# Performance work log

Measured on AMD Instinct MI355X. Metric: run time of the kernel, lower is better.

Reference implementation:

```python
import jax, jax.numpy as jnp
import numpy as np

B, S, E, H = 2, 2048, 1024, 16
DK = E // H
THRESHOLD = 0.1


def setup_inputs() -> dict:
    key = jax.random.key(0)
    ks = jax.random.split(key, 11)
    s = 1.0 / np.sqrt(E)
    return {
        "queries": jax.random.normal(ks[0], (B, S, E), jnp.float32),
        "keys": jax.random.normal(ks[1], (B, S, E), jnp.float32),
        "values": jax.random.normal(ks[2], (B, S, E), jnp.float32),
        "Wq": jax.random.normal(ks[3], (E, E), jnp.float32) * s,
        "bq": jnp.zeros((E,), jnp.float32),
        "Wk": jax.random.normal(ks[4], (E, E), jnp.float32) * s,
        "bk": jnp.zeros((E,), jnp.float32),
        "Wv": jax.random.normal(ks[5], (E, E), jnp.float32) * s,
        "bv": jnp.zeros((E,), jnp.float32),
        "Wp": jax.random.normal(ks[6], (E, E), jnp.float32) * s,
        "bp": jnp.zeros((E,), jnp.float32),
    }


def _split(x):
    # [B,S,E] -> [B,H,S,dk]
    return x.reshape(B, S, H, DK).transpose(0, 2, 1, 3)


def reference(queries, keys, values, Wq, bq, Wk, bk, Wv, bv, Wp, bp):
    q = _split(queries @ Wq.T + bq)
    k = _split(keys @ Wk.T + bk)
    v = _split(values @ Wv.T + bv)
    logits = jnp.einsum("bhsd,bhtd->bhst", q, k) / np.sqrt(DK)
    probs = jax.nn.softmax(logits, axis=-1)                    # [B,H,S,S]
    mask = (probs > THRESHOLD).astype(probs.dtype)
    # straight-through: value = mask*probs, grads flow via (mask*probs + probs)
    thr = mask * probs - jax.lax.stop_gradient(probs) + probs
    hidden = jnp.einsum("bhst,bhtd->bhsd", thr, v)             # [B,H,S,dk]
    merged = hidden.transpose(0, 2, 1, 3).reshape(B, S, E)
    out = merged @ Wp.T + bp
    adjacency = probs.mean(axis=1)                             # avg_attn_heads=True
    return (out, adjacency)
```

## Files before the change

### kernel.cpp

```cpp
#include <hip/hip_runtime.h>
#include <cstddef>
#include <cstdint>

constexpr size_t OUT_ELEMS = (size_t)2 * 2048 * 1024;

typedef _Float16 f16_t;
typedef __attribute__((ext_vector_type(8))) _Float16 f16x8;
typedef __attribute__((ext_vector_type(4))) float f32x4;

#define SCL2      0.1803368801111204f
#define LOG2_0P1  -3.3219280948873623f

#define EXP2F(x)  __builtin_amdgcn_exp2f(x)
#define LOG2F(x)  __builtin_amdgcn_logf(x)

#define WAITV(N)  asm volatile("s_waitcnt vmcnt(" #N ")" ::: "memory")
__device__ __forceinline__ void ringbar() {
    __builtin_amdgcn_s_barrier();
    __builtin_amdgcn_sched_barrier(0);
}

__device__ __forceinline__ f32x4 mfma16(f16x8 a, f16x8 b, f32x4 c) {
    return __builtin_amdgcn_mfma_f32_16x16x32_f16(a, b, c, 0, 0, 0);
}

__device__ __forceinline__ void gload16(const void* g, void* l) {
    __builtin_amdgcn_global_load_lds(
        (const __attribute__((address_space(1))) void*)g,
        (__attribute__((address_space(3))) void*)l, 16, 0, 0);
}

__global__ __launch_bounds__(256)
void prep_kernel(const float4* __restrict__ q, const float4* __restrict__ k,
                 const float4* __restrict__ v, const float4* __restrict__ wq,
                 const float4* __restrict__ wk, const float4* __restrict__ wv,
                 const float4* __restrict__ wp,
                 unsigned short* __restrict__ xq, unsigned short* __restrict__ xk,
                 unsigned short* __restrict__ xv, unsigned short* __restrict__ wqh,
                 unsigned short* __restrict__ wkh, unsigned short* __restrict__ wvh,
                 unsigned short* __restrict__ wph)
{
    const int z = blockIdx.y;
    const int i = blockIdx.x * 256 + threadIdx.x;
    const float4* src; unsigned short* dst; int total4;
    switch (z) {
        case 0:  src = q;  dst = xq;  total4 = 1048576; break;
        case 1:  src = k;  dst = xk;  total4 = 1048576; break;
        case 2:  src = v;  dst = xv;  total4 = 1048576; break;
        case 3:  src = wq; dst = wqh; total4 = 262144;  break;
        case 4:  src = wk; dst = wkh; total4 = 262144;  break;
        case 5:  src = wv; dst = wvh; total4 = 262144;  break;
        default: src = wp; dst = wph; total4 = 262144;  break;
    }
    if (i >= total4) return;
    const float4 v4 = src[i];
    const float vv[4] = {v4.x, v4.y, v4.z, v4.w};
    unsigned short u[4];
#pragma unroll
    for (int j = 0; j < 4; ++j) {
        f16_t h = (f16_t)vv[j];
        u[j] = __builtin_bit_cast(unsigned short, h);
    }
    uint2 w;
    w.x = u[0] | ((unsigned)u[1] << 16); w.y = u[2] | ((unsigned)u[3] << 16);
    *(uint2*)(dst + (size_t)i * 4) = w;
}

template<int OUTMODE>
__global__ __launch_bounds__(512)
void gemm_mfma(const f16_t* __restrict__ A, const f16_t* __restrict__ B,
               const float* __restrict__ bias, float scaleB,
               float* __restrict__ outF, f16_t* __restrict__ outB,
               const unsigned* __restrict__ dmask)
{
    __shared__ __align__(16) char Asl[3][16384];
    __shared__ __align__(16) char Bsl[3][16384];

    const int tid = threadIdx.x;
    const int lane = tid & 63;
    const int w = tid >> 6;
    const int wm = w >> 1;
    const int wn = w & 1;
    const int n0 = blockIdx.x * 128;
    const int m0 = blockIdx.y * 128;

    if (OUTMODE == 2) {
        const int bb = m0 >> 11;
        const int st0 = (m0 & 2047) >> 6;
        unsigned dd = 0;
        for (int hh = 0; hh < 16; ++hh)
            dd |= dmask[(bb * 16 + hh) * 32 + st0] | dmask[(bb * 16 + hh) * 32 + st0 + 1];
        if (dd == 0u) {
            const int row = tid >> 2;
            const int c0 = (tid & 3) * 32;
            float* dst = outF + (size_t)(m0 + row) * 1024 + n0 + c0;
#pragma unroll
            for (int j = 0; j < 8; ++j)
                *(float4*)(dst + j * 4) = *(const float4*)(bias + n0 + c0 + j * 4);
            return;
        }
    }

    f32x4 acc[2][4] = {};

    auto stage = [&](int ki, int buf) {
        const int kt = ki * 64;
#pragma unroll
        for (int inst = 0; inst < 2; ++inst) {
            int L = inst * 8192 + tid * 16;
            int row = L >> 7;
            int k16 = ((L >> 4) & 7) ^ (row & 7);
            gload16(A + (size_t)(m0 + row) * 1024 + kt + k16 * 8,
                    Asl[buf] + inst * 8192 + w * 1024);
            gload16(B + (size_t)(n0 + row) * 1024 + kt + k16 * 8,
                    Bsl[buf] + inst * 8192 + w * 1024);
        }
    };

    stage(0, 0);

    for (int ki = 0; ki < 16; ++ki) {
        if (ki + 1 < 16) stage(ki + 1, (ki + 1) % 3);
        if (ki < 15) { WAITV(4); } else { WAITV(0); }
        ringbar();
        const char* Ab = Asl[ki % 3];
        const char* Bb = Bsl[ki % 3];
#pragma unroll
        for (int kf = 0; kf < 2; ++kf) {
            const int k16 = kf * 4 + (lane >> 4);
            f16x8 af[2], bfr[4];
#pragma unroll
            for (int mi = 0; mi < 2; ++mi) {
                int row = wm * 32 + mi * 16 + (lane & 15);
                af[mi] = *(const f16x8*)(Ab + (row << 7) + ((k16 ^ (row & 7)) << 4));
            }
#pragma unroll
            for (int ni = 0; ni < 4; ++ni) {
                int row = wn * 64 + ni * 16 + (lane & 15);
                bfr[ni] = *(const f16x8*)(Bb + (row << 7) + ((k16 ^ (row & 7)) << 4));
            }
#pragma unroll
            for (int mi = 0; mi < 2; ++mi)
#pragma unroll
                for (int ni = 0; ni < 4; ++ni)
                    acc[mi][ni] = mfma16(af[mi], bfr[ni], acc[mi][ni]);
        }
    }

    const int crow0 = wm * 32 + (lane >> 4) * 4;
    const int ccol0 = wn * 64 + (lane & 15);
#pragma unroll
    for (int mi = 0; mi < 2; ++mi) {
#pragma unroll
        for (int ni = 0; ni < 4; ++ni) {
            const int n = n0 + ccol0 + ni * 16;
            const float bb = bias[n];
            if (OUTMODE == 2) {
#pragma unroll
                for (int r = 0; r < 4; ++r) {
                    const int m = m0 + crow0 + mi * 16 + r;
                    outF[(size_t)m * 1024 + n] = acc[mi][ni][r] + bb;
                }
            } else if (OUTMODE == 0) {
                const int h = n >> 6, d = n & 63;
#pragma unroll
                for (int r = 0; r < 4; ++r) {
                    const int m = m0 + crow0 + mi * 16 + r;
                    const int b = m >> 11, s = m & 2047;
                    const float v = acc[mi][ni][r] + bb;
                    const size_t idx = ((size_t)(b * 16 + h) * 2048 + s) * 64 + d;
                    outB[idx] = (f16_t)(v * scaleB);
                    outF[idx] = v;
                }
            } else {
                const int h = n >> 6, d = n & 63;
                const int m = m0 + crow0 + mi * 16;
                const int b = m >> 11, s = m & 2047;
                unsigned short us[4];
#pragma unroll
                for (int r = 0; r < 4; ++r) {
                    f16_t t = (f16_t)(acc[mi][ni][r] + bb);
                    us[r] = __builtin_bit_cast(unsigned short, t);
                }
                uint2 pk;
                pk.x = us[0] | ((unsigned)us[1] << 16);
                pk.y = us[2] | ((unsigned)us[3] << 16);
                *(uint2*)(outB + ((size_t)(b * 16 + h) * 64 + d) * 2048 + s) = pk;
            }
        }
    }
}

__global__ __launch_bounds__(512)
void attn_zsweep_kernel(const f16_t* __restrict__ qh, const f16_t* __restrict__ kh,
                        float2* __restrict__ partials)
{
    __shared__ __align__(16) char Klds[16384];

    const int tid = threadIdx.x;
    const int lane = tid & 63;
    const int g = lane >> 4;
    const int w = tid >> 6;
    const int tc = blockIdx.x;
    const int bh = blockIdx.y;

    {
        const size_t kbase = ((size_t)bh * 2048 + tc * 128) * 64;
#pragma unroll
        for (int inst = 0; inst < 2; ++inst) {
            int L = inst * 8192 + tid * 16;
            int row = L >> 7;
            int k16 = ((L >> 4) & 7) ^ (row & 7);
            gload16(kh + kbase + (size_t)row * 64 + k16 * 8,
                    Klds + inst * 8192 + w * 1024);
        }
    }
    __syncthreads();

    auto qload = [&](int si, f16x8& a, f16x8& b) {
        const size_t rb = ((size_t)bh * 2048 + si * 128 + w * 16 + (lane & 15)) * 64;
        a = *(const f16x8*)(qh + rb + g * 8);
        b = *(const f16x8*)(qh + rb + 32 + g * 8);
    };

    auto compute = [&](int si, f16x8 q0, f16x8 q1) {
        f32x4 acc[8] = {};
#pragma unroll
        for (int kf = 0; kf < 2; ++kf) {
            const f16x8 qf = kf ? q1 : q0;
            const int k16 = kf * 4 + g;
#pragma unroll
            for (int tg = 0; tg < 8; ++tg) {
                const int t = tg * 16 + (lane & 15);
                f16x8 bfr = *(const f16x8*)(Klds + (t << 7) + ((k16 ^ (t & 7)) << 4));
                acc[tg] = mfma16(qf, bfr, acc[tg]);
            }
        }
#pragma unroll
        for (int r = 0; r < 4; ++r) {
            float sm = 0.0f, mx = -1e30f;
#pragma unroll
            for (int tg = 0; tg < 8; ++tg) {
                const float l2 = acc[tg][r];
                sm += EXP2F(l2);
                mx = fmaxf(mx, l2);
            }
#pragma unroll
            for (int mk = 1; mk < 16; mk <<= 1) {
                sm += __shfl_xor(sm, mk);
                mx = fmaxf(mx, __shfl_xor(mx, mk));
            }
            if ((lane & 15) == 0) {
                const int srow = si * 128 + w * 16 + g * 4 + r;
                partials[((size_t)bh * 2048 + srow) * 16 + tc] = make_float2(sm, mx);
            }
        }
    };

    f16x8 qA0, qA1, qB0, qB1;
    qload(0, qA0, qA1);
    for (int si = 0; si < 16; si += 2) {
        qload(si + 1, qB0, qB1);
        compute(si, qA0, qA1);
        if (si + 2 < 16) qload(si + 2, qA0, qA1);
        compute(si + 1, qB0, qB1);
    }
}

__global__ __launch_bounds__(256)
void zred_kernel(const float2* __restrict__ partials, float* __restrict__ stats,
                 unsigned* __restrict__ dirtymask)
{
    const int tid = threadIdx.x;
    const int bh = blockIdx.y;
    const int s = blockIdx.x * 256 + tid;
    const float4* p = (const float4*)(partials + ((size_t)bh * 2048 + s) * 16);
    float sm = 0.0f, mx = -1e30f;
#pragma unroll
    for (int i = 0; i < 8; ++i) {
        const float4 v = p[i];
        sm += v.x + v.z;
        mx = fmaxf(mx, fmaxf(v.y, v.w));
    }
    const float lgZ = LOG2F(sm);
    stats[(size_t)bh * 2048 + s] = lgZ;
    const bool dirty = mx > lgZ + LOG2_0P1 - 0.10f;
    const unsigned long long m = __ballot(dirty);
    if ((tid & 63) == 0)
        dirtymask[bh * 32 + (s >> 6)] = (m != 0ull) ? 1u : 0u;
}

__global__ __launch_bounds__(256)
void attn_pv_kernel(const f16_t* __restrict__ qh, const f16_t* __restrict__ kh,
                    const f16_t* __restrict__ vT,
                    const float* __restrict__ qf32, const float* __restrict__ kf32,
                    const float* __restrict__ stats, const unsigned* __restrict__ dirtymask,
                    const float2* __restrict__ partials,
                    f16_t* __restrict__ merged)
{
    __shared__ __align__(16) char Klds[8192];
    __shared__ __align__(16) char Vlds[8192];
    __shared__ __align__(16) char Pl[4][2048];
    __shared__ unsigned cflags;

    const int tid = threadIdx.x;
    const int lane = tid & 63;
    const int g = lane >> 4;
    const int w = tid >> 6;
    const int s0 = blockIdx.x * 64;
    const int bh = blockIdx.y;
    const int b = bh >> 4, h = bh & 15;

    if (dirtymask[bh * 32 + blockIdx.x] == 0u) {
        const int row = s0 + (tid >> 2);
        f16_t* dst = merged + ((size_t)b * 2048 + row) * 1024 + h * 64 + (tid & 3) * 16;
        const uint4 z = {0u, 0u, 0u, 0u};
        *(uint4*)dst = z;
        *(uint4*)(dst + 8) = z;
        return;
    }

    f16x8 qf[2];
    float lgZ[4], lthr[4];
    {
        const size_t rowbase = ((size_t)bh * 2048 + s0 + w * 16 + (lane & 15)) * 64;
        qf[0] = *(const f16x8*)(qh + rowbase + g * 8);
        qf[1] = *(const f16x8*)(qh + rowbase + 32 + g * 8);
#pragma unroll
        for (int r = 0; r < 4; ++r) {
            lgZ[r] = stats[(size_t)bh * 2048 + s0 + w * 16 + g * 4 + r];
            lthr[r] = lgZ[r] + LOG2_0P1;
        }
    }

    if (tid == 0) cflags = 0u;
    __syncthreads();
    {
        unsigned f = 0;
#pragma unroll
        for (int r = 0; r < 4; ++r) {
            const size_t rowg = (size_t)bh * 2048 + s0 + w * 16 + g * 4 + r;
            const float thr = lthr[r] - 0.10f;
#pragma unroll
            for (int tc = 0; tc < 16; ++tc)
                if (partials[rowg * 16 + tc].y > thr) f |= (1u << tc);
        }
        if (f) atomicOr(&cflags, f);
    }
    __syncthreads();
    const unsigned flags = cflags;

    const size_t kbase = (size_t)bh * 2048 * 64;
    const size_t vbase = (size_t)bh * 64 * 2048;

    f32x4 hacc[4] = {};
    for (int tcc = 0; tcc < 2048; tcc += 64) {
        if (!((flags >> (tcc >> 7)) & 1u)) continue;
#pragma unroll
        for (int inst = 0; inst < 2; ++inst) {
            int L = inst * 4096 + tid * 16;
            int t = L >> 7;
            int k16 = ((L >> 4) & 7) ^ (t & 7);
            gload16(kh + kbase + (size_t)(tcc + t) * 64 + k16 * 8,
                    Klds + inst * 4096 + w * 1024);
            int d = t;
            gload16(vT + vbase + (size_t)d * 2048 + tcc + k16 * 8,
                    Vlds + inst * 4096 + w * 1024);
        }
        __syncthreads();

        f32x4 acc[4] = {};
#pragma unroll
        for (int kf = 0; kf < 2; ++kf) {
            const int k16 = kf * 4 + g;
            f16x8 bfr[4];
#pragma unroll
            for (int tg = 0; tg < 4; ++tg) {
                int t = tg * 16 + (lane & 15);
                bfr[tg] = *(const f16x8*)(Klds + (t << 7) + ((k16 ^ (t & 7)) << 4));
            }
#pragma unroll
            for (int tg = 0; tg < 4; ++tg)
                acc[tg] = mfma16(qf[kf], bfr[tg], acc[tg]);
        }

        char* pb = Pl[w];
        bool any = false;
#pragma unroll
        for (int tg = 0; tg < 4; ++tg)
#pragma unroll
            for (int r = 0; r < 4; ++r) {
                const float l2 = acc[tg][r];
                float p = 0.0f;
                if (l2 > lthr[r] - 0.07f) {
                    if (fabsf(l2 - lthr[r]) < 0.07f) {
                        const float* qr = qf32 + ((size_t)bh * 2048 + s0 + w * 16 + g * 4 + r) * 64;
                        const float* kr = kf32 + ((size_t)bh * 2048 + tcc + tg * 16 + (lane & 15)) * 64;
                        float dt = 0.0f;
                        for (int dd = 0; dd < 64; ++dd) dt += qr[dd] * kr[dd];
                        const float pe = EXP2F(dt * SCL2 - lgZ[r]);
                        p = (pe > 0.1f) ? pe : 0.0f;
                    } else {
                        p = EXP2F(l2 - lgZ[r]);
                    }
                }
                any |= (p != 0.0f);
                const int row = g * 4 + r;
                const int t = tg * 16 + (lane & 15);
                *(f16_t*)(pb + (row << 7) + ((2 * t) ^ ((row & 7) << 4))) = (f16_t)p;
            }

        if (__ballot(any) != 0ull) {
#pragma unroll
            for (int kf = 0; kf < 2; ++kf) {
                const int t16 = kf * 4 + g;
                f16x8 pa, vb[4];
                {
                    const int row = lane & 15;
                    pa = *(const f16x8*)(pb + (row << 7) + ((t16 ^ (row & 7)) << 4));
                }
#pragma unroll
                for (int ni = 0; ni < 4; ++ni) {
                    const int d = ni * 16 + (lane & 15);
                    vb[ni] = *(const f16x8*)(Vlds + (d << 7) + ((t16 ^ (d & 7)) << 4));
                }
#pragma unroll
                for (int ni = 0; ni < 4; ++ni)
                    hacc[ni] = mfma16(pa, vb[ni], hacc[ni]);
            }
        }
        __syncthreads();
    }

#pragma unroll
    for (int ni = 0; ni < 4; ++ni)
#pragma unroll
        for (int r = 0; r < 4; ++r) {
            const int srow = s0 + w * 16 + g * 4 + r;
            const int col = h * 64 + ni * 16 + (lane & 15);
            merged[((size_t)b * 2048 + srow) * 1024 + col] = (f16_t)hacc[ni][r];
        }
}

__global__ __launch_bounds__(256, 4)
void attn_adj_kernel(const f16_t* __restrict__ qh, const f16_t* __restrict__ kh,
                     const float* __restrict__ stats, float* __restrict__ adj)
{
    __shared__ __align__(16) char Klds[2][16384];
    __shared__ __align__(16) float Sl[16 * 64];

    const int tid = threadIdx.x;
    const int lane = tid & 63;
    const int g = lane >> 4;
    const int w = tid >> 6;
    const int t0 = blockIdx.x * 128;
    const int s0 = blockIdx.y * 64;
    const int b  = blockIdx.z;

    {
        const int hh = tid >> 4;
        const int sl = (tid * 4) & 63;
        const float4 v = *(const float4*)(stats + ((size_t)(b * 16 + hh) * 2048 + s0 + sl));
        *(float4*)&Sl[tid * 4] = v;
    }

    auto stageK = [&](int h, int buf) {
        const size_t kbase = ((size_t)(b * 16 + h) * 2048 + t0) * 64;
#pragma unroll
        for (int inst = 0; inst < 4; ++inst) {
            int L = inst * 4096 + tid * 16;
            int row = L >> 7;
            int k16 = ((L >> 4) & 7) ^ (row & 7);
            gload16(kh + kbase + (size_t)row * 64 + k16 * 8,
                    Klds[buf] + inst * 4096 + w * 1024);
        }
    };
    auto qload = [&](int h, f16x8& a, f16x8& bq) {
        const size_t rb = ((size_t)(b * 16 + h) * 2048 + s0 + w * 16 + (lane & 15)) * 64;
        a  = *(const f16x8*)(qh + rb + g * 8);
        bq = *(const f16x8*)(qh + rb + 32 + g * 8);
    };

    f32x4 aacc[8] = {};

    auto body = [&](int h, f16x8 q0, f16x8 q1) {
        float cc[4];
#pragma unroll
        for (int r = 0; r < 4; ++r)
            cc[r] = Sl[h * 64 + w * 16 + g * 4 + r] + 4.0f;
        const char* Kb = Klds[h & 1];
        f32x4 acc[8] = {};
#pragma unroll
        for (int kf = 0; kf < 2; ++kf) {
            const f16x8 qf = kf ? q1 : q0;
            const int k16 = kf * 4 + g;
#pragma unroll
            for (int tg = 0; tg < 8; ++tg) {
                const int t = tg * 16 + (lane & 15);
                const f16x8 bfr = *(const f16x8*)(Kb + (t << 7) + ((k16 ^ (t & 7)) << 4));
                acc[tg] = mfma16(qf, bfr, acc[tg]);
            }
        }
#pragma unroll
        for (int tg = 0; tg < 8; ++tg)
#pragma unroll
            for (int r = 0; r < 4; ++r)
                aacc[tg][r] += EXP2F(acc[tg][r] - cc[r]);
    };

    f16x8 qA0, qA1, qB0, qB1;
    stageK(0, 0);
    qload(0, qA0, qA1);
    __syncthreads();

    for (int h = 0; h < 16; h += 2) {
        if (h + 1 < 16) { stageK(h + 1, (h + 1) & 1); qload(h + 1, qB0, qB1); }
        body(h, qA0, qA1);
        __syncthreads();
        if (h + 2 < 16) { stageK(h + 2, (h + 2) & 1); qload(h + 2, qA0, qA1); }
        body(h + 1, qB0, qB1);
        __syncthreads();
    }

#pragma unroll
    for (int tg = 0; tg < 8; ++tg)
#pragma unroll
        for (int r = 0; r < 4; ++r) {
            const int s = s0 + w * 16 + g * 4 + r;
            adj[((size_t)b * 2048 + s) * 2048 + t0 + tg * 16 + (lane & 15)] = aacc[tg][r];
        }
}

extern "C" void kernel_launch(void* const* d_in, const int* in_sizes, int n_in,
                              void* d_out, int out_size, void* d_ws, size_t ws_size,
                              hipStream_t stream)
{
    (void)in_sizes; (void)n_in; (void)out_size; (void)ws_size;

    const float* queries = (const float*)d_in[0];
    const float* keys    = (const float*)d_in[1];
    const float* values  = (const float*)d_in[2];
    const float* Wq = (const float*)d_in[3];
    const float* bq = (const float*)d_in[4];
    const float* Wk = (const float*)d_in[5];
    const float* bk = (const float*)d_in[6];
    const float* Wv = (const float*)d_in[7];
    const float* bv = (const float*)d_in[8];
    const float* Wp = (const float*)d_in[9];
    const float* bp = (const float*)d_in[10];

    float* out = (float*)d_out;
    float* adj = out + OUT_ELEMS;

    char* ws = (char*)d_ws;
    f16_t* Xq   = (f16_t*)(ws);
    f16_t* Xk   = (f16_t*)(ws + 8388608);
    f16_t* Xv   = (f16_t*)(ws + 16777216);
    f16_t* Wqh  = (f16_t*)(ws + 25165824);
    f16_t* Wkh  = (f16_t*)(ws + 27262976);
    f16_t* Wvh  = (f16_t*)(ws + 29360128);
    f16_t* Wph  = (f16_t*)(ws + 31457280);
    f16_t* qh16 = (f16_t*)(ws + 33554432);
    f16_t* kh16 = (f16_t*)(ws + 41943040);
    f16_t* vT   = (f16_t*)(ws + 50331648);
    f16_t* mg   = (f16_t*)(ws + 58720256);
    float* qf32 = (float*)(ws + 67108864);
    float* kf32 = (float*)(ws + 83886080);
    float* stats = (float*)(ws + 100663296);
    float2* partials  = (float2*)(ws);
    unsigned* dirtymask = (unsigned*)(ws + 16777216 + 4194304);

    prep_kernel<<<dim3(4096, 7), 256, 0, stream>>>(
        (const float4*)queries, (const float4*)keys, (const float4*)values,
        (const float4*)Wq, (const float4*)Wk, (const float4*)Wv, (const float4*)Wp,
        (unsigned short*)Xq, (unsigned short*)Xk, (unsigned short*)Xv,
        (unsigned short*)Wqh, (unsigned short*)Wkh, (unsigned short*)Wvh,
        (unsigned short*)Wph);

    const dim3 gg(8, 32);
    gemm_mfma<0><<<gg, 512, 0, stream>>>(Xq, Wqh, bq, SCL2, qf32, qh16, nullptr);
    gemm_mfma<0><<<gg, 512, 0, stream>>>(Xk, Wkh, bk, 1.0f, kf32, kh16, nullptr);
    gemm_mfma<1><<<gg, 512, 0, stream>>>(Xv, Wvh, bv, 1.0f, nullptr, vT, nullptr);

    attn_zsweep_kernel<<<dim3(16, 32), 512, 0, stream>>>(qh16, kh16, partials);
    zred_kernel<<<dim3(8, 32), 256, 0, stream>>>(partials, stats, dirtymask);
    attn_pv_kernel<<<dim3(32, 32), 256, 0, stream>>>(qh16, kh16, vT, qf32, kf32,
                                                     stats, dirtymask, partials, mg);
    attn_adj_kernel<<<dim3(16, 32, 2), 256, 0, stream>>>(qh16, kh16, stats, adj);

    gemm_mfma<2><<<gg, 512, 0, stream>>>(mg, Wph, bp, 1.0f, out, nullptr, dirtymask);
}
```

Baseline: 168.8 us.

## Batch Q/K projection GEMMs in one launch and use double-buffered LDS

The Q and K projection GEMMs now run as one launch, using blockIdx.z to pick the second operand set. This removes one kernel launch and gives the GPU twice as many blocks at once. The GEMM's LDS pipeline also drops from a three-slot ring with manual vmcnt waits to a two-slot double buffer guarded by __syncthreads. That cuts shared memory per block from 96KB to 64KB, which may let more blocks share a CU. The cost is a full barrier and wait each k-step, so global loads overlap less with MFMA work.

```diff
diff --git a/kernel.cpp b/kernel.cpp
--- a/kernel.cpp
+++ b/kernel.cpp
@@ -13,12 +13,6 @@
 
 #define EXP2F(x)  __builtin_amdgcn_exp2f(x)
 #define LOG2F(x)  __builtin_amdgcn_logf(x)
-
-#define WAITV(N)  asm volatile("s_waitcnt vmcnt(" #N ")" ::: "memory")
-__device__ __forceinline__ void ringbar() {
-    __builtin_amdgcn_s_barrier();
-    __builtin_amdgcn_sched_barrier(0);
-}
 
 __device__ __forceinline__ f32x4 mfma16(f16x8 a, f16x8 b, f32x4 c) {
     return __builtin_amdgcn_mfma_f32_16x16x32_f16(a, b, c, 0, 0, 0);
@@ -71,10 +65,13 @@
 void gemm_mfma(const f16_t* __restrict__ A, const f16_t* __restrict__ B,
                const float* __restrict__ bias, float scaleB,
                float* __restrict__ outF, f16_t* __restrict__ outB,
-               const unsigned* __restrict__ dmask)
-{
-    __shared__ __align__(16) char Asl[3][16384];
-    __shared__ __align__(16) char Bsl[3][16384];
+               const unsigned* __restrict__ dmask,
+               const f16_t* A2 = nullptr, const f16_t* B2 = nullptr,
+               const float* bias2 = nullptr, float scaleB2 = 1.0f,
+               float* outF2 = nullptr, f16_t* outB2 = nullptr)
+{
+    __shared__ __align__(16) char Asl[2][16384];
+    __shared__ __align__(16) char Bsl[2][16384];
 
     const int tid = threadIdx.x;
     const int lane = tid & 63;
@@ -83,6 +80,10 @@
     const int wn = w & 1;
     const int n0 = blockIdx.x * 128;
     const int m0 = blockIdx.y * 128;
+
+    if (OUTMODE == 0 && blockIdx.z == 1) {
+        A = A2; B = B2; bias = bias2; scaleB = scaleB2; outF = outF2; outB = outB2;
+    }
 
     if (OUTMODE == 2) {
         const int bb = m0 >> 11;
@@ -118,13 +119,12 @@
     };
 
     stage(0, 0);
+    __syncthreads();
 
     for (int ki = 0; ki < 16; ++ki) {
-        if (ki + 1 < 16) stage(ki + 1, (ki + 1) % 3);
-        if (ki < 15) { WAITV(4); } else { WAITV(0); }
-        ringbar();
-        const char* Ab = Asl[ki % 3];
-        const char* Bb = Bsl[ki % 3];
+        if (ki + 1 < 16) stage(ki + 1, (ki + 1) & 1);
+        const char* Ab = Asl[ki & 1];
+        const char* Bb = Bsl[ki & 1];
 #pragma unroll
         for (int kf = 0; kf < 2; ++kf) {
             const int k16 = kf * 4 + (lane >> 4);
@@ -145,6 +145,7 @@
                 for (int ni = 0; ni < 4; ++ni)
                     acc[mi][ni] = mfma16(af[mi], bfr[ni], acc[mi][ni]);
         }
+        if (ki + 1 < 16) __syncthreads();
     }
 
     const int crow0 = wm * 32 + (lane >> 4) * 4;
@@ -577,10 +578,10 @@
         (unsigned short*)Wqh, (unsigned short*)Wkh, (unsigned short*)Wvh,
         (unsigned short*)Wph);
 
-    const dim3 gg(8, 32);
-    gemm_mfma<0><<<gg, 512, 0, stream>>>(Xq, Wqh, bq, SCL2, qf32, qh16, nullptr);
-    gemm_mfma<0><<<gg, 512, 0, stream>>>(Xk, Wkh, bk, 1.0f, kf32, kh16, nullptr);
-    gemm_mfma<1><<<gg, 512, 0, stream>>>(Xv, Wvh, bv, 1.0f, nullptr, vT, nullptr);
+    gemm_mfma<0><<<dim3(8, 32, 2), 512, 0, stream>>>(
+        Xq, Wqh, bq, SCL2, qf32, qh16, nullptr,
+        Xk, Wkh, bk, 1.0f, kf32, kh16);
+    gemm_mfma<1><<<dim3(8, 32), 512, 0, stream>>>(Xv, Wvh, bv, 1.0f, nullptr, vT, nullptr);
 
     attn_zsweep_kernel<<<dim3(16, 32), 512, 0, stream>>>(qh16, kh16, partials);
     zred_kernel<<<dim3(8, 32), 256, 0, stream>>>(partials, stats, dirtymask);
@@ -588,5 +589,5 @@
                                                      stats, dirtymask, partials, mg);
     attn_adj_kernel<<<dim3(16, 32, 2), 256, 0, stream>>>(qh16, kh16, stats, adj);
 
-    gemm_mfma<2><<<gg, 512, 0, stream>>>(mg, Wph, bp, 1.0f, out, nullptr, dirtymask);
-}
+    gemm_mfma<2><<<dim3(8, 32), 512, 0, stream>>>(mg, Wph, bp, 1.0f, out, nullptr, dirtymask);
+}
```

After: 178.8 us. +5.9%, slower.
